# Kernel optimization log

Hardware: AMD Instinct MI355X
Metric: run time of the kernel (lower is better)

The kernel has to match this reference:

```python
import jax, jax.numpy as jnp
import numpy as np

NEG = -10000.0


def _build_label_vocab():
    vocab = {'O': 0}
    i = 1
    for t in ['PER', 'ORG', 'LOC', 'MISC']:
        for p in ['B', 'I', 'E', 'S']:
            vocab[f'{p}-{t}'] = i
            i += 1
    return vocab


def _init_transition(key):
    """Random transition with BIOES constraints, matching CRF.initialize()."""
    vocab = _build_label_vocab()
    L = len(vocab) + 2          # 19 (17 labels + start + end)
    start, end = L - 2, L - 1
    T = np.array(jax.random.normal(key, (L, L)), dtype=np.float32)
    T[:, end] = NEG
    T[start, :] = NEG
    for lf, i_f in vocab.items():
        pf, tf = ('O', 'O') if lf == 'O' else lf.split('-')
        for lt, i_t in vocab.items():
            pt, tt = ('O', 'O') if lt == 'O' else lt.split('-')
            allowed = (pf in ('O', 'E', 'S') and pt in ('O', 'B', 'S')) or \
                      (pf in ('B', 'I') and pt in ('I', 'E') and tf == tt)
            if not allowed:
                T[i_t, i_f] = NEG
    return jnp.asarray(T)


def setup_inputs() -> dict:
    key = jax.random.key(0)
    k1, k2, k3, k4 = jax.random.split(key, 4)
    B, S, NL = 4096, 256, 17
    logits = jax.random.normal(k1, (B, S, NL), dtype=jnp.float32)
    labels = jax.random.randint(k2, (B, S), 0, NL)
    lens = jax.random.randint(k3, (B,), 1, S + 1)   # lengths in [1, S]
    transition = _init_transition(k4)                # [19, 19]
    return {"logits": logits, "labels": labels, "lens": lens,
            "transition": transition}


def reference(logits, labels, lens, transition):
    """CRF log-likelihood: gold_score(pad_logits(logits)) - norm_score."""
    B, S, NL = logits.shape
    L = transition.shape[0]       # label_size = NL + 2
    start, end = L - 2, L - 1

    # pad_logits: append start/end columns with -10000
    pads = jnp.full((B, S, 2), NEG, dtype=logits.dtype)
    logits_p = jnp.concatenate([logits, pads], axis=2)   # [B, S, L]

    tmask = (jnp.arange(S)[None, :] < lens[:, None])     # [B, S] valid tokens

    # ---- gold score ----
    # unary: gather emission score of the gold label at each position
    unary = jnp.take_along_axis(logits_p, labels[:, :, None], axis=2)[:, :, 0]
    unary = (unary * tmask.astype(logits.dtype)).sum(axis=1)

    # binary: transition scores along the gold path (with start/end padding)
    labels_ext = jnp.concatenate(
        [jnp.full((B, 1), start, labels.dtype), labels,
         jnp.full((B, 1), end, labels.dtype)], axis=1)   # [B, S+2]
    emask = jnp.arange(S + 2)[None, :] < (lens + 1)[:, None]
    labels_ext = jnp.where(emask, labels_ext, end)
    trn_scr = transition[labels_ext[:, 1:], labels_ext[:, :-1]]  # [B, S+1]
    bmask = (jnp.arange(S + 1)[None, :] < (lens + 1)[:, None]).astype(logits.dtype)
    binary = (trn_scr * bmask).sum(axis=1)

    gold = unary + binary

    # ---- partition (norm) score: forward algorithm over time ----
    alpha0 = jnp.full((B, L), NEG, dtype=logits.dtype).at[:, start].set(0.0)

    def step(alpha, xs):
        logit, m = xs  # logit: [B, L], m: [B] bool (position < len)
        # alpha_nxt[b,i] = logit[b,i] + LSE_j(alpha[b,j] + T[i,j])
        nxt = logit + jax.nn.logsumexp(alpha[:, None, :] + transition[None], axis=2)
        alpha = jnp.where(m[:, None], nxt, alpha)
        return alpha, None

    alpha, _ = jax.lax.scan(step, alpha0,
                            (jnp.swapaxes(logits_p, 0, 1), tmask.T))
    alpha = alpha + transition[end][None, :]
    norm = jax.nn.logsumexp(alpha, axis=1)

    return gold - norm   # [B] per-sequence log-likelihood
```

## Files before the change

kernel.cpp:

```cpp
#include <hip/hip_runtime.h>

constexpr int S   = 256;
constexpr int NL  = 17;
constexpr int L   = 19;
constexpr int WPB = 2;

__global__ __launch_bounds__(64 * WPB)
void crf_fwd(const float* __restrict__ logits,
             const int*   __restrict__ labels,
             const int*   __restrict__ lens,
             const float* __restrict__ transition,
             float* __restrict__ out, int totalElemM1)
{
    __shared__ float Tsh[L * L];
    __shared__ __align__(16) float pbuf[WPB][2][2][32];

    const int tid  = threadIdx.x;
    const int wave = tid >> 6;
    const int wtid = tid & 63;
    const int half = wtid >> 5;
    const int lane = wtid & 31;
    const int b    = blockIdx.x * WPB + wave;

    for (int k = tid; k < L * L; k += 64 * WPB) Tsh[k] = transition[k];
    __syncthreads();

    const int  i    = lane;
    const bool act  = (i < L);
    const bool emit = (i < NL);
    const int  ic   = act ? i : 0;

    float coef[L];
    #pragma unroll
    for (int j = 0; j < L; ++j)
        coef[j] = __expf(half ? Tsh[j * L + ic] : Tsh[ic * L + j]);

    const int len = lens[b];
    const int mid = len >> 1;
    const int nb  = len - 1 - mid;
    const int nup = half ? nb : mid;
    const int nsteps = (mid + 7) & ~7;

    const int seqbase = b * (S * NL);

    float p = act ? __expf(half ? Tsh[(L - 1) * L + ic]
                                : Tsh[ic * L + (L - 2)])
                  : 0.0f;
    float m = 0.0f;

    const char* lgbase = (const char*)logits;
    const int capHiF = 4 * min(seqbase + (S - 1) * NL + i, totalElemM1);
    const int capHi  = half ? 0x7ffffffc : capHiF;
    const int capLo  = half ? 4 * (seqbase + i) : 0;
    const int stride = half ? -(8 * NL * 4) : (8 * NL * 4);

    int   off[8];
    float lgbuf[8];
    #pragma unroll
    for (int u = 0; u < 8; ++u) {
        int tok = half ? (len - 1 - u) : u;
        tok = tok > 0 ? tok : 0;
        int o = 4 * (seqbase + tok * NL + i);
        o = min(o, capHiF);
        off[u] = o;
        lgbuf[u] = *(const float*)(lgbase + o);
    }

    for (int tb = 0; tb < nsteps; tb += 8) {
        #pragma unroll
        for (int u = 0; u < 8; ++u) {
            const int   t  = tb + u;
            const float lg = lgbuf[u];
            int o = off[u] + stride;
            o = max(o, capLo);
            o = min(o, capHi);
            off[u] = o;
            lgbuf[u] = *(const float*)(lgbase + o);

            const bool upd = (t < nup);

            const float el = emit ? __expf(lg) : 0.0f;
            const float pe = p * el;

            float* pb = &pbuf[wave][half][u & 1][0];
            pb[i] = pe;
            asm volatile("" ::: "memory");
            const float4* q = (const float4*)pb;
            const float4 q0 = q[0], q1 = q[1], q2 = q[2], q3 = q[3], q4 = q[4];

            float a0 = q0.x * coef[0];
            float a1 = q0.y * coef[1];
            float a2 = q0.z * coef[2];
            float a3 = q0.w * coef[3];
            a0 = fmaf(q1.x, coef[4],  a0);
            a1 = fmaf(q1.y, coef[5],  a1);
            a2 = fmaf(q1.z, coef[6],  a2);
            a3 = fmaf(q1.w, coef[7],  a3);
            a0 = fmaf(q2.x, coef[8],  a0);
            a1 = fmaf(q2.y, coef[9],  a1);
            a2 = fmaf(q2.z, coef[10], a2);
            a3 = fmaf(q2.w, coef[11], a3);
            a0 = fmaf(q3.x, coef[12], a0);
            a1 = fmaf(q3.y, coef[13], a1);
            a2 = fmaf(q3.z, coef[14], a2);
            a3 = fmaf(q3.w, coef[15], a3);
            a0 = fmaf(q4.x, coef[16], a0);
            a1 = fmaf(q4.y, coef[17], a1);
            a2 = fmaf(q4.z, coef[18], a2);

            float pn = (a0 + a1) + (a2 + a3);

            if ((u & 3) == 3) {
                float m0 = fmaxf(fmaxf(q0.x, q0.y), fmaxf(q0.z, q0.w));
                float m1 = fmaxf(fmaxf(q1.x, q1.y), fmaxf(q1.z, q1.w));
                float m2 = fmaxf(fmaxf(q2.x, q2.y), fmaxf(q2.z, q2.w));
                float m3 = fmaxf(fmaxf(q3.x, q3.y), fmaxf(q3.z, q3.w));
                float m4 = fmaxf(fmaxf(q4.x, q4.y), q4.z);
                float mx = fmaxf(fmaxf(m0, m1), fmaxf(fmaxf(m2, m3), m4));
                pn *= __frcp_rn(mx);
                m += upd ? __logf(mx) : 0.0f;
            }
            p = upd ? pn : p;
        }
    }

    {
        float lgf = 0.0f;
        if (half && emit) lgf = logits[(size_t)(seqbase + mid * NL + i)];
        if (half) p = emit ? p * __expf(lgf) : 0.0f;
    }

    const float other = __shfl_xor(p, 32);
    float prod = act ? p * other : 0.0f;
    #pragma unroll
    for (int o = 16; o >= 1; o >>= 1) prod += __shfl_xor(prod, o, 32);
    const float mtot = m + __shfl_xor(m, 32);
    const float norm = mtot + __logf(prod);

    const int* labp = labels + b * S;
    float gsum = 0.0f;
    for (int c = 0; c < len; c += 64) {
        const int tok = c + wtid;
        if (tok < len) {
            const int lab = labp[tok];
            const int prv = (tok == 0) ? (L - 2) : labp[tok - 1];
            gsum += logits[(size_t)(seqbase + tok * NL + lab)] + Tsh[lab * L + prv];
        }
    }
    #pragma unroll
    for (int o = 32; o >= 1; o >>= 1) gsum += __shfl_xor(gsum, o);
    const float gold = gsum + Tsh[(L - 1) * L + labp[len - 1]];

    if (wtid == 0) out[b] = gold - norm;
}

extern "C" void kernel_launch(void* const* d_in, const int* in_sizes, int n_in,
                              void* d_out, int out_size, void* d_ws, size_t ws_size,
                              hipStream_t stream)
{
    (void)n_in; (void)out_size; (void)d_ws; (void)ws_size;
    const float* logits     = (const float*)d_in[0];
    const int*   labels     = (const int*)d_in[1];
    const int*   lens       = (const int*)d_in[2];
    const float* transition = (const float*)d_in[3];
    float*       out        = (float*)d_out;
    const int B = in_sizes[2];
    const int totalElemM1 = B * S * NL - 1;
    crf_fwd<<<dim3(B / WPB), dim3(64 * WPB), 0, stream>>>(
        logits, labels, lens, transition, out, totalElemM1);
}
```

Before: 136.1 us.

## Sort sequences by length and use persistent waves with atomic work queue

Adds a single-block prep kernel that counting-sorts batch indices by descending length into a global buffer. The main kernel becomes persistent: a fixed grid of waves pulls sequence indices from an atomic counter, processing longest sequences first. The aim is to balance load across CUs so short sequences fill gaps left by long ones, reducing tail imbalance. It adds an extra serial launch, per-wave atomics, and the sorted buffer indirection.

Result: slower. 194.6 us (+43.0%).

```diff
diff --git a/kernel.cpp b/kernel.cpp
--- a/kernel.cpp
+++ b/kernel.cpp
@@ -4,13 +4,53 @@
 constexpr int NL  = 17;
 constexpr int L   = 19;
 constexpr int WPB = 2;
+constexpr int NB  = 1536;
+constexpr int CAP = 16384;
+
+__device__ int g_sorted[CAP];
+__device__ int g_counter;
+
+__global__ __launch_bounds__(1024)
+void crf_prep(const int* __restrict__ lens, int B, int nwaves)
+{
+    __shared__ int hist[256];
+    __shared__ int offs[256];
+    const int tid = threadIdx.x;
+    if (tid == 0) g_counter = nwaves;
+    if (B > CAP) return;
+    if (tid < 256) hist[tid] = 0;
+    __syncthreads();
+    for (int b = tid; b < B; b += 1024) {
+        int k = 256 - lens[b];
+        k = k < 0 ? 0 : (k > 255 ? 255 : k);
+        atomicAdd(&hist[k], 1);
+    }
+    __syncthreads();
+    int cnt = 0;
+    if (tid < 256) cnt = hist[tid];
+    for (int d = 1; d < 256; d <<= 1) {
+        int v = 0;
+        if (tid < 256) { v = hist[tid]; if (tid >= d) v += hist[tid - d]; }
+        __syncthreads();
+        if (tid < 256) hist[tid] = v;
+        __syncthreads();
+    }
+    if (tid < 256) offs[tid] = hist[tid] - cnt;
+    __syncthreads();
+    for (int b = tid; b < B; b += 1024) {
+        int k = 256 - lens[b];
+        k = k < 0 ? 0 : (k > 255 ? 255 : k);
+        int pos = atomicAdd(&offs[k], 1);
+        g_sorted[pos] = b;
+    }
+}
 
 __global__ __launch_bounds__(64 * WPB)
 void crf_fwd(const float* __restrict__ logits,
              const int*   __restrict__ labels,
              const int*   __restrict__ lens,
              const float* __restrict__ transition,
-             float* __restrict__ out, int totalElemM1)
+             float* __restrict__ out, int totalElemM1, int B, int useSort)
 {
     __shared__ float Tsh[L * L];
     __shared__ __align__(16) float pbuf[WPB][2][2][32];
@@ -20,7 +60,6 @@
     const int wtid = tid & 63;
     const int half = wtid >> 5;
     const int lane = wtid & 31;
-    const int b    = blockIdx.x * WPB + wave;
 
     for (int k = tid; k < L * L; k += 64 * WPB) Tsh[k] = transition[k];
     __syncthreads();
@@ -35,123 +74,137 @@
     for (int j = 0; j < L; ++j)
         coef[j] = __expf(half ? Tsh[j * L + ic] : Tsh[ic * L + j]);
 
-    const int len = lens[b];
-    const int mid = len >> 1;
-    const int nb  = len - 1 - mid;
-    const int nup = half ? nb : mid;
-    const int nsteps = (mid + 7) & ~7;
-
-    const int seqbase = b * (S * NL);
-
-    float p = act ? __expf(half ? Tsh[(L - 1) * L + ic]
-                                : Tsh[ic * L + (L - 2)])
-                  : 0.0f;
-    float m = 0.0f;
-
+    const float p0 = act ? __expf(half ? Tsh[(L - 1) * L + ic]
+                                       : Tsh[ic * L + (L - 2)])
+                         : 0.0f;
+    const int   stride = half ? -(8 * NL * 4) : (8 * NL * 4);
     const char* lgbase = (const char*)logits;
-    const int capHiF = 4 * min(seqbase + (S - 1) * NL + i, totalElemM1);
-    const int capHi  = half ? 0x7ffffffc : capHiF;
-    const int capLo  = half ? 4 * (seqbase + i) : 0;
-    const int stride = half ? -(8 * NL * 4) : (8 * NL * 4);
-
-    int   off[8];
-    float lgbuf[8];
-    #pragma unroll
-    for (int u = 0; u < 8; ++u) {
-        int tok = half ? (len - 1 - u) : u;
-        tok = tok > 0 ? tok : 0;
-        int o = 4 * (seqbase + tok * NL + i);
-        o = min(o, capHiF);
-        off[u] = o;
-        lgbuf[u] = *(const float*)(lgbase + o);
-    }
-
-    for (int tb = 0; tb < nsteps; tb += 8) {
+
+    int idx = blockIdx.x * WPB + wave;
+
+    while (idx < B) {
+        const int b = useSort ? g_sorted[idx] : idx;
+
+        const int len = lens[b];
+        const int mid = len >> 1;
+        const int nb  = len - 1 - mid;
+        const int nup = half ? nb : mid;
+        const int nsteps = (mid + 7) & ~7;
+
+        const int seqbase = b * (S * NL);
+
+        float p = p0;
+        float m = 0.0f;
+
+        const int capHiF = 4 * min(seqbase + (S - 1) * NL + i, totalElemM1);
+        const int capHi  = half ? 0x7ffffffc : capHiF;
+        const int capLo  = half ? 4 * (seqbase + i) : 0;
+
+        int   off[8];
+        float lgbuf[8];
         #pragma unroll
         for (int u = 0; u < 8; ++u) {
-            const int   t  = tb + u;
-            const float lg = lgbuf[u];
-            int o = off[u] + stride;
-            o = max(o, capLo);
-            o = min(o, capHi);
+            int tok = half ? (len - 1 - u) : u;
+            tok = tok > 0 ? tok : 0;
+            int o = 4 * (seqbase + tok * NL + i);
+            o = min(o, capHiF);
             off[u] = o;
             lgbuf[u] = *(const float*)(lgbase + o);
-
-            const bool upd = (t < nup);
-
-            const float el = emit ? __expf(lg) : 0.0f;
-            const float pe = p * el;
-
-            float* pb = &pbuf[wave][half][u & 1][0];
-            pb[i] = pe;
-            asm volatile("" ::: "memory");
-            const float4* q = (const float4*)pb;
-            const float4 q0 = q[0], q1 = q[1], q2 = q[2], q3 = q[3], q4 = q[4];
-
-            float a0 = q0.x * coef[0];
-            float a1 = q0.y * coef[1];
-            float a2 = q0.z * coef[2];
-            float a3 = q0.w * coef[3];
-            a0 = fmaf(q1.x, coef[4],  a0);
-            a1 = fmaf(q1.y, coef[5],  a1);
-            a2 = fmaf(q1.z, coef[6],  a2);
-            a3 = fmaf(q1.w, coef[7],  a3);
-            a0 = fmaf(q2.x, coef[8],  a0);
-            a1 = fmaf(q2.y, coef[9],  a1);
-            a2 = fmaf(q2.z, coef[10], a2);
-            a3 = fmaf(q2.w, coef[11], a3);
-            a0 = fmaf(q3.x, coef[12], a0);
-            a1 = fmaf(q3.y, coef[13], a1);
-            a2 = fmaf(q3.z, coef[14], a2);
-            a3 = fmaf(q3.w, coef[15], a3);
-            a0 = fmaf(q4.x, coef[16], a0);
-            a1 = fmaf(q4.y, coef[17], a1);
-            a2 = fmaf(q4.z, coef[18], a2);
-
-            float pn = (a0 + a1) + (a2 + a3);
-
-            if ((u & 3) == 3) {
-                float m0 = fmaxf(fmaxf(q0.x, q0.y), fmaxf(q0.z, q0.w));
-                float m1 = fmaxf(fmaxf(q1.x, q1.y), fmaxf(q1.z, q1.w));
-                float m2 = fmaxf(fmaxf(q2.x, q2.y), fmaxf(q2.z, q2.w));
-                float m3 = fmaxf(fmaxf(q3.x, q3.y), fmaxf(q3.z, q3.w));
-                float m4 = fmaxf(fmaxf(q4.x, q4.y), q4.z);
-                float mx = fmaxf(fmaxf(m0, m1), fmaxf(fmaxf(m2, m3), m4));
-                pn *= __frcp_rn(mx);
-                m += upd ? __logf(mx) : 0.0f;
+        }
+
+        for (int tb = 0; tb < nsteps; tb += 8) {
+            #pragma unroll
+            for (int u = 0; u < 8; ++u) {
+                const int   t  = tb + u;
+                const float lg = lgbuf[u];
+                int o = off[u] + stride;
+                o = max(o, capLo);
+                o = min(o, capHi);
+                off[u] = o;
+                lgbuf[u] = *(const float*)(lgbase + o);
+
+                const bool upd = (t < nup);
+
+                const float el = emit ? __expf(lg) : 0.0f;
+                const float pe = p * el;
+
+                float* pb = &pbuf[wave][half][u & 1][0];
+                pb[i] = pe;
+                asm volatile("" ::: "memory");
+                const float4* q = (const float4*)pb;
+                const float4 q0 = q[0], q1 = q[1], q2 = q[2], q3 = q[3], q4 = q[4];
+
+                float a0 = q0.x * coef[0];
+                float a1 = q0.y * coef[1];
+                float a2 = q0.z * coef[2];
+                float a3 = q0.w * coef[3];
+                a0 = fmaf(q1.x, coef[4],  a0);
+                a1 = fmaf(q1.y, coef[5],  a1);
+                a2 = fmaf(q1.z, coef[6],  a2);
+                a3 = fmaf(q1.w, coef[7],  a3);
+                a0 = fmaf(q2.x, coef[8],  a0);
+                a1 = fmaf(q2.y, coef[9],  a1);
+                a2 = fmaf(q2.z, coef[10], a2);
+                a3 = fmaf(q2.w, coef[11], a3);
+                a0 = fmaf(q3.x, coef[12], a0);
+                a1 = fmaf(q3.y, coef[13], a1);
+                a2 = fmaf(q3.z, coef[14], a2);
+                a3 = fmaf(q3.w, coef[15], a3);
+                a0 = fmaf(q4.x, coef[16], a0);
+                a1 = fmaf(q4.y, coef[17], a1);
+                a2 = fmaf(q4.z, coef[18], a2);
+
+                float pn = (a0 + a1) + (a2 + a3);
+
+                if ((u & 3) == 3) {
+                    float m0 = fmaxf(fmaxf(q0.x, q0.y), fmaxf(q0.z, q0.w));
+                    float m1 = fmaxf(fmaxf(q1.x, q1.y), fmaxf(q1.z, q1.w));
+                    float m2 = fmaxf(fmaxf(q2.x, q2.y), fmaxf(q2.z, q2.w));
+                    float m3 = fmaxf(fmaxf(q3.x, q3.y), fmaxf(q3.z, q3.w));
+                    float m4 = fmaxf(fmaxf(q4.x, q4.y), q4.z);
+                    float mx = fmaxf(fmaxf(m0, m1), fmaxf(fmaxf(m2, m3), m4));
+                    pn *= __frcp_rn(mx);
+                    m += upd ? __logf(mx) : 0.0f;
+                }
+                p = upd ? pn : p;
             }
-            p = upd ? pn : p;
-        }
-    }
-
-    {
-        float lgf = 0.0f;
-        if (half && emit) lgf = logits[(size_t)(seqbase + mid * NL + i)];
-        if (half) p = emit ? p * __expf(lgf) : 0.0f;
-    }
-
-    const float other = __shfl_xor(p, 32);
-    float prod = act ? p * other : 0.0f;
-    #pragma unroll
-    for (int o = 16; o >= 1; o >>= 1) prod += __shfl_xor(prod, o, 32);
-    const float mtot = m + __shfl_xor(m, 32);
-    const float norm = mtot + __logf(prod);
-
-    const int* labp = labels + b * S;
-    float gsum = 0.0f;
-    for (int c = 0; c < len; c += 64) {
-        const int tok = c + wtid;
-        if (tok < len) {
-            const int lab = labp[tok];
-            const int prv = (tok == 0) ? (L - 2) : labp[tok - 1];
-            gsum += logits[(size_t)(seqbase + tok * NL + lab)] + Tsh[lab * L + prv];
-        }
-    }
-    #pragma unroll
-    for (int o = 32; o >= 1; o >>= 1) gsum += __shfl_xor(gsum, o);
-    const float gold = gsum + Tsh[(L - 1) * L + labp[len - 1]];
-
-    if (wtid == 0) out[b] = gold - norm;
+        }
+
+        {
+            float lgf = 0.0f;
+            if (half && emit) lgf = logits[(size_t)(seqbase + mid * NL + i)];
+            if (half) p = emit ? p * __expf(lgf) : 0.0f;
+        }
+
+        const float other = __shfl_xor(p, 32);
+        float prod = act ? p * other : 0.0f;
+        #pragma unroll
+        for (int o = 16; o >= 1; o >>= 1) prod += __shfl_xor(prod, o, 32);
+        const float mtot = m + __shfl_xor(m, 32);
+        const float norm = mtot + __logf(prod);
+
+        const int* labp = labels + b * S;
+        float gsum = 0.0f;
+        for (int c = 0; c < len; c += 64) {
+            const int tok = c + wtid;
+            if (tok < len) {
+                const int lab = labp[tok];
+                const int prv = (tok == 0) ? (L - 2) : labp[tok - 1];
+                gsum += logits[(size_t)(seqbase + tok * NL + lab)] + Tsh[lab * L + prv];
+            }
+        }
+        #pragma unroll
+        for (int o = 32; o >= 1; o >>= 1) gsum += __shfl_xor(gsum, o);
+        const float gold = gsum + Tsh[(L - 1) * L + labp[len - 1]];
+
+        if (wtid == 0) out[b] = gold - norm;
+
+        if (wtid == 0) {
+            int c = *(volatile int*)&g_counter;
+            idx = (c >= B) ? B : atomicAdd(&g_counter, 1);
+        }
+        idx = __shfl(idx, 0);
+    }
 }
 
 extern "C" void kernel_launch(void* const* d_in, const int* in_sizes, int n_in,
@@ -166,6 +219,10 @@
     float*       out        = (float*)d_out;
     const int B = in_sizes[2];
     const int totalElemM1 = B * S * NL - 1;
-    crf_fwd<<<dim3(B / WPB), dim3(64 * WPB), 0, stream>>>(
-        logits, labels, lens, transition, out, totalElemM1);
+    const int useSort = (B <= CAP) ? 1 : 0;
+    const int nwaves  = NB * WPB;
+
+    crf_prep<<<dim3(1), dim3(1024), 0, stream>>>(lens, B, nwaves);
+    crf_fwd<<<dim3(NB), dim3(64 * WPB), 0, stream>>>(
+        logits, labels, lens, transition, out, totalElemM1, B, useSort);
 }
```
